# Kernel optimization log

Hardware: AMD Instinct MI355X
Metric: run time of the kernel (lower is better)

## Reference

```python
import jax, jax.numpy as jnp
import numpy as np

NUM_NODES = 100000
NUM_EDGES = 3200000
NUM_GRAPHS = 512
IN_DIM, OUT_DIM = 128, 16
DIMS = [IN_DIM, 32, 48, 64]


def glorot(key, shape):
    lim = float(np.sqrt(6.0 / (shape[0] + shape[1])))
    return jax.random.uniform(key, shape, jnp.float32, -lim, lim)


def setup_inputs() -> dict:
    key = jax.random.key(0)
    ks = jax.random.split(key, 12)
    x = jax.random.normal(ks[0], (NUM_NODES, IN_DIM), jnp.float32)
    edge_index = jax.random.randint(ks[1], (2, NUM_EDGES), 0, NUM_NODES, jnp.int64)
    batch = jnp.sort(jax.random.randint(ks[2], (NUM_NODES,), 0, NUM_GRAPHS, jnp.int64))
    params = {}
    for i in range(3):
        params[f"W{i+1}"] = glorot(ks[3 + i], (DIMS[i], DIMS[i + 1]))
        params[f"b{i+1}"] = jnp.zeros((DIMS[i + 1],), jnp.float32)
    params["fc1_w"] = glorot(ks[6], (64, 32))
    params["fc1_b"] = jnp.zeros((32,), jnp.float32)
    params["fc2_w"] = glorot(ks[7], (32, OUT_DIM))
    params["fc2_b"] = jnp.zeros((OUT_DIM,), jnp.float32)
    return {"x": x, "edge_index": edge_index, "batch": batch, **params}


def gcn_conv(x, W, b, src, dst, deg_inv_sqrt):
    # h = x @ W; aggregate with symmetric normalization + self loops (PyG GCNConv)
    h = x @ W  # [N, out]
    norm = deg_inv_sqrt[src] * deg_inv_sqrt[dst]  # [E]
    msg = h[src] * norm[:, None]  # [E, out]  (gather)
    agg = jnp.zeros_like(h).at[dst].add(msg)  # scatter-add to targets
    self_loop = h * (deg_inv_sqrt * deg_inv_sqrt)[:, None]
    return agg + self_loop + b


def reference(x, edge_index, batch, W1, b1, W2, b2, W3, b3, fc1_w, fc1_b, fc2_w, fc2_b):
    src, dst = edge_index[0], edge_index[1]
    n = x.shape[0]
    # degree with self loops: deg[i] = in-degree + 1
    deg = jnp.zeros((n,), jnp.float32).at[dst].add(1.0) + 1.0
    dis = jax.lax.rsqrt(deg)
    h = jax.nn.relu(gcn_conv(x, W1, b1, src, dst, dis))
    h = jax.nn.relu(gcn_conv(h, W2, b2, src, dst, dis))
    h = jax.nn.relu(gcn_conv(h, W3, b3, src, dst, dis))
    # global mean pool per graph
    sums = jax.ops.segment_sum(h, batch, num_segments=NUM_GRAPHS)
    cnts = jax.ops.segment_sum(jnp.ones((n,), jnp.float32), batch, num_segments=NUM_GRAPHS)
    pooled = sums / jnp.maximum(cnts, 1.0)[:, None]  # [G, 64]
    z = jax.nn.relu(pooled @ fc1_w + fc1_b)
    logits = z @ fc2_w + fc2_b
    return jax.nn.softmax(logits, axis=1)
```

## Files before the change

### kernel.cpp

```cpp
#include <hip/hip_runtime.h>
#include <hip/hip_fp16.h>

static constexpr int NN = 100000;
static constexpr int NE = 3200000;
static constexpr int NG = 512;
static constexpr int NCB = 196;
static constexpr int CHK = 8192;
static constexpr int NCH = (NE + CHK - 1) / CHK;
static constexpr int NCNT = NCB * NCH;
static constexpr int SCAN_BLK = 2048;
static constexpr int NSB = (NCNT + SCAN_BLK - 1) / SCAN_BLK;

typedef float f32x2 __attribute__((ext_vector_type(2)));

__device__ __forceinline__ void set2_fp8x4(unsigned v, f32x2* a) {
    a[0] = __builtin_amdgcn_cvt_pk_f32_fp8((int)v, false);
    a[1] = __builtin_amdgcn_cvt_pk_f32_fp8((int)v, true);
}
__device__ __forceinline__ void acc2_fp8x4(unsigned v, f32x2* a) {
    a[0] += __builtin_amdgcn_cvt_pk_f32_fp8((int)v, false);
    a[1] += __builtin_amdgcn_cvt_pk_f32_fp8((int)v, true);
}
__device__ __forceinline__ unsigned pack_fp8x4(float a, float b, float c, float d) {
    int p = __builtin_amdgcn_cvt_pk_fp8_f32(a, b, 0, false);
    p = __builtin_amdgcn_cvt_pk_fp8_f32(c, d, p, true);
    return (unsigned)p;
}
__device__ __forceinline__ unsigned pkh2(float a, float b) {
    __half2 h = __floats2half2_rn(a, b);
    return *(unsigned*)&h;
}

__global__ __launch_bounds__(256) void k_histC(const int4* __restrict__ dst4,
                                               int* __restrict__ cntC, int e4) {
    __shared__ int h[NCB];
    for (int i = threadIdx.x; i < NCB; i += 256) h[i] = 0;
    __syncthreads();
    const int s4 = blockIdx.x * (CHK / 4), e4end = min(s4 + CHK / 4, e4);
    for (int i = s4 + threadIdx.x; i < e4end; i += 256) {
        int4 d = dst4[i];
        atomicAdd(&h[d.x >> 9], 1);
        atomicAdd(&h[d.y >> 9], 1);
        atomicAdd(&h[d.z >> 9], 1);
        atomicAdd(&h[d.w >> 9], 1);
    }
    __syncthreads();
    for (int i = threadIdx.x; i < NCB; i += 256)
        cntC[(size_t)i * NCH + blockIdx.x] = h[i];
}

__global__ __launch_bounds__(256) void k_scanA(const int* __restrict__ in,
                                               int* __restrict__ out,
                                               int* __restrict__ bsum, int n) {
    __shared__ int s[256];
    const int tid = threadIdx.x;
    const int base = blockIdx.x * SCAN_BLK + tid * 8;
    int v[8], t = 0;
#pragma unroll
    for (int c = 0; c < 8; c++) {
        int idx = base + c;
        v[c] = (idx < n) ? in[idx] : 0;
        t += v[c];
    }
    s[tid] = t;
    __syncthreads();
    for (int off = 1; off < 256; off <<= 1) {
        int x = (tid >= off) ? s[tid - off] : 0;
        __syncthreads();
        s[tid] += x;
        __syncthreads();
    }
    if (tid == 255) bsum[blockIdx.x] = s[255];
    int run = s[tid] - t;
#pragma unroll
    for (int c = 0; c < 8; c++) {
        int idx = base + c;
        if (idx < n) out[idx] = run;
        run += v[c];
    }
}

__global__ __launch_bounds__(256) void k_scanB(int* __restrict__ bsum, int nb) {
    __shared__ int s[256];
    const int tid = threadIdx.x;
    int v = (tid < nb) ? bsum[tid] : 0;
    s[tid] = v;
    __syncthreads();
    for (int off = 1; off < 256; off <<= 1) {
        int x = (tid >= off) ? s[tid - off] : 0;
        __syncthreads();
        s[tid] += x;
        __syncthreads();
    }
    if (tid < nb) bsum[tid] = s[tid] - v;
}

__global__ __launch_bounds__(256) void k_scatC(const int4* __restrict__ src4,
                                               const int4* __restrict__ dst4,
                                               const int* __restrict__ sc,
                                               const int* __restrict__ bsum,
                                               unsigned* __restrict__ tmp, int e4) {
    __shared__ int cur[NCB];
    for (int i = threadIdx.x; i < NCB; i += 256) {
        size_t idx = (size_t)i * NCH + blockIdx.x;
        cur[i] = sc[idx] + bsum[idx >> 11];
    }
    __syncthreads();
    const int s4 = blockIdx.x * (CHK / 4), e4end = min(s4 + CHK / 4, e4);
    for (int i = s4 + threadIdx.x; i < e4end; i += 256) {
        int4 d = dst4[i];
        int4 sv = src4[i];
        int p0 = atomicAdd(&cur[d.x >> 9], 1);
        tmp[p0] = ((unsigned)(d.x & 511) << 17) | (unsigned)sv.x;
        int p1 = atomicAdd(&cur[d.y >> 9], 1);
        tmp[p1] = ((unsigned)(d.y & 511) << 17) | (unsigned)sv.y;
        int p2 = atomicAdd(&cur[d.z >> 9], 1);
        tmp[p2] = ((unsigned)(d.z & 511) << 17) | (unsigned)sv.z;
        int p3 = atomicAdd(&cur[d.w >> 9], 1);
        tmp[p3] = ((unsigned)(d.w & 511) << 17) | (unsigned)sv.w;
    }
}

__global__ __launch_bounds__(1024) void k_fill512(const unsigned* __restrict__ tmp,
                                                  const int* __restrict__ sc,
                                                  const int* __restrict__ bsum,
                                                  int* __restrict__ csr,
                                                  int* __restrict__ degi,
                                                  int* __restrict__ offs,
                                                  float* __restrict__ dis,
                                                  int n, int etotal) {
    __shared__ int cnt[512];
    __shared__ int s[512];
    __shared__ int cur[512];
    const int b = blockIdx.x, tid = threadIdx.x;
    if (tid < 512) cnt[tid] = 0;
    size_t i0 = (size_t)b * NCH;
    const int e0 = sc[i0] + bsum[i0 >> 11];
    int e1 = etotal;
    if (b + 1 < NCB) {
        size_t i1 = (size_t)(b + 1) * NCH;
        e1 = sc[i1] + bsum[i1 >> 11];
    }
    __syncthreads();
    for (int e = e0 + tid; e < e1; e += 1024)
        atomicAdd(&cnt[tmp[e] >> 17], 1);
    __syncthreads();
    int v = 0;
    if (tid < 512) { v = cnt[tid]; s[tid] = v; }
    __syncthreads();
    for (int off = 1; off < 512; off <<= 1) {
        int x = 0;
        if (tid < 512 && tid >= off) x = s[tid - off];
        __syncthreads();
        if (tid < 512) s[tid] += x;
        __syncthreads();
    }
    if (tid < 512) {
        int c = e0 + s[tid] - v;
        cur[tid] = c;
        int node = b * 512 + tid;
        if (node < n) {
            degi[node] = v;
            offs[node] = c;
            dis[node] = rsqrtf((float)v + 1.0f);
        }
    }
    __syncthreads();
    for (int e = e0 + tid; e < e1; e += 1024) {
        unsigned pk = tmp[e];
        int p = atomicAdd(&cur[pk >> 17], 1);
        csr[p] = (int)(pk & 0x1FFFFu);
    }
}

__global__ __launch_bounds__(256) void k_gemm1(const float* __restrict__ X,
                                               const float* __restrict__ W,
                                               const float* __restrict__ dis,
                                               unsigned* __restrict__ H, int n) {
    constexpr int IN = 128, ROWS = 32;
    __shared__ float sW[IN * 32];
    __shared__ float sX[ROWS][IN];
    const int tid = threadIdx.x;
    for (int i = tid; i < IN * 32; i += 256) sW[i] = W[i];
    const int row0 = blockIdx.x * ROWS;
    const float4* X4 = (const float4*)X;
    for (int i = tid; i < ROWS * 32; i += 256) {
        int r = row0 + (i >> 5);
        float4 v = make_float4(0.f, 0.f, 0.f, 0.f);
        if (r < n) v = X4[(size_t)r * 32 + (i & 31)];
        ((float4*)&sX[i >> 5][0])[i & 31] = v;
    }
    __syncthreads();
    const int lr = tid >> 3;
    const int cg = tid & 7;
    const int gr = row0 + lr;
    float acc[4] = {0.f, 0.f, 0.f, 0.f};
#pragma unroll 8
    for (int k = 0; k < IN; k++) {
        float xv = sX[lr][k];
#pragma unroll
        for (int c = 0; c < 4; c++)
            acc[c] = fmaf(xv, sW[k * 32 + 4 * cg + c], acc[c]);
    }
    if (gr < n) {
        float dd = dis[gr];
        H[(size_t)gr * 8 + cg] =
            pack_fp8x4(acc[0] * dd, acc[1] * dd, acc[2] * dd, acc[3] * dd);
    }
}

__global__ __launch_bounds__(256) void k_pull2(
        const uint2* __restrict__ Hp, const int* __restrict__ offs,
        const int* __restrict__ degi, const int* __restrict__ csr,
        const float* __restrict__ dis, const float* __restrict__ b,
        uint2* __restrict__ A, int n) {
    const int group = threadIdx.x >> 2, j0 = threadIdx.x & 3;
    const int d = blockIdx.x * 64 + group;
    if (d >= n) return;
    f32x2 acc[4];
    uint2 sv = Hp[(size_t)d * 4 + j0];
    set2_fp8x4(sv.x, acc); set2_fp8x4(sv.y, acc + 2);
    int e = offs[d];
    const int end = e + degi[d];
    for (; e < end; e += 8) {
        uint2 v[8];
#pragma unroll
        for (int i = 0; i < 8; i++) {
            int ee = e + i;
            int idx = csr[min(ee, NE - 1)];
            uint2 t = Hp[(size_t)idx * 4 + j0];
            if (ee >= end) { t.x = 0u; t.y = 0u; }
            v[i] = t;
        }
#pragma unroll
        for (int i = 0; i < 8; i++) {
            acc2_fp8x4(v[i].x, acc); acc2_fp8x4(v[i].y, acc + 2);
        }
    }
    const float dd = dis[d];
    float r[8];
#pragma unroll
    for (int c = 0; c < 4; c++) {
        r[2 * c]     = fmaxf(fmaf(acc[c].x, dd, b[8 * j0 + 2 * c]), 0.f) * dd;
        r[2 * c + 1] = fmaxf(fmaf(acc[c].y, dd, b[8 * j0 + 2 * c + 1]), 0.f) * dd;
    }
    A[(size_t)d * 4 + j0] = make_uint2(pack_fp8x4(r[0], r[1], r[2], r[3]),
                                       pack_fp8x4(r[4], r[5], r[6], r[7]));
}

__global__ __launch_bounds__(256) void k_pullmm32(
        const uint2* __restrict__ Hp, const int* __restrict__ offs,
        const int* __restrict__ degi, const int* __restrict__ csr,
        const float* __restrict__ dis, const float* __restrict__ W,
        const float* __restrict__ b, unsigned* __restrict__ A, int n) {
    __shared__ float sW[32 * 48];
    __shared__ float rows[64][33];
    for (int i = threadIdx.x; i < 32 * 48; i += 256) sW[i] = W[i];
    const int group = threadIdx.x >> 2, j0 = threadIdx.x & 3;
    const int d = blockIdx.x * 64 + group;
    if (d < n) {
        f32x2 acc[4];
        uint2 sv = Hp[(size_t)d * 4 + j0];
        set2_fp8x4(sv.x, acc); set2_fp8x4(sv.y, acc + 2);
        int e = offs[d];
        const int end = e + degi[d];
        for (; e < end; e += 8) {
            uint2 v[8];
#pragma unroll
            for (int i = 0; i < 8; i++) {
                int ee = e + i;
                int idx = csr[min(ee, NE - 1)];
                uint2 t = Hp[(size_t)idx * 4 + j0];
                if (ee >= end) { t.x = 0u; t.y = 0u; }
                v[i] = t;
            }
#pragma unroll
            for (int i = 0; i < 8; i++) {
                acc2_fp8x4(v[i].x, acc); acc2_fp8x4(v[i].y, acc + 2);
            }
        }
        const float dd = dis[d];
#pragma unroll
        for (int c = 0; c < 4; c++) {
            rows[group][8 * j0 + 2 * c]     = acc[c].x * dd;
            rows[group][8 * j0 + 2 * c + 1] = acc[c].y * dd;
        }
    }
    __syncthreads();
    const int row0 = blockIdx.x * 64;
    const int nl = threadIdx.x & 63, cgb = threadIdx.x >> 6;
    const int gr = row0 + nl;
    if (gr < n) {
        const float4* sW4 = (const float4*)sW;
        float s[3][4];
#pragma unroll
        for (int o = 0; o < 3; o++)
#pragma unroll
            for (int c = 0; c < 4; c++) s[o][c] = b[12 * cgb + 4 * o + c];
#pragma unroll 8
        for (int k = 0; k < 32; k++) {
            float rv = rows[nl][k];
#pragma unroll
            for (int o = 0; o < 3; o++) {
                float4 w = sW4[k * 12 + cgb * 3 + o];
                s[o][0] = fmaf(rv, w.x, s[o][0]);
                s[o][1] = fmaf(rv, w.y, s[o][1]);
                s[o][2] = fmaf(rv, w.z, s[o][2]);
                s[o][3] = fmaf(rv, w.w, s[o][3]);
            }
        }
        const float dd2 = dis[gr];
#pragma unroll
        for (int o = 0; o < 3; o++) {
            float r0 = fmaxf(s[o][0], 0.f) * dd2;
            float r1 = fmaxf(s[o][1], 0.f) * dd2;
            float r2 = fmaxf(s[o][2], 0.f) * dd2;
            float r3 = fmaxf(s[o][3], 0.f) * dd2;
            A[(size_t)gr * 12 + cgb * 3 + o] = pack_fp8x4(r0, r1, r2, r3);
        }
    }
}

__global__ __launch_bounds__(256) void k_pullmm48(
        const uint4* __restrict__ Hp,
        const int* __restrict__ offs,
        const int* __restrict__ degi, const int* __restrict__ csr,
        const float* __restrict__ dis, const float* __restrict__ W,
        const float* __restrict__ b, __half* __restrict__ A, int n) {
    __shared__ float sW[48 * 64];
    __shared__ float rows[64][49];
    for (int i = threadIdx.x; i < 48 * 64; i += 256) sW[i] = W[i];
    const int group = threadIdx.x >> 2, j0 = threadIdx.x & 3;
    const int d = blockIdx.x * 64 + group;
    if (d < n && j0 < 3) {
        f32x2 acc[8];
        uint4 sv = Hp[(size_t)d * 3 + j0];
        set2_fp8x4(sv.x, acc);     set2_fp8x4(sv.y, acc + 2);
        set2_fp8x4(sv.z, acc + 4); set2_fp8x4(sv.w, acc + 6);
        int e = offs[d];
        const int end = e + degi[d];
        for (; e < end; e += 8) {
            uint4 v[8];
#pragma unroll
            for (int i = 0; i < 8; i++) {
                int ee = e + i;
                int idx = csr[min(ee, NE - 1)];
                uint4 t = Hp[(size_t)idx * 3 + j0];
                if (ee >= end) { t.x = 0u; t.y = 0u; t.z = 0u; t.w = 0u; }
                v[i] = t;
            }
#pragma unroll
            for (int i = 0; i < 8; i++) {
                acc2_fp8x4(v[i].x, acc);     acc2_fp8x4(v[i].y, acc + 2);
                acc2_fp8x4(v[i].z, acc + 4); acc2_fp8x4(v[i].w, acc + 6);
            }
        }
        const float dd = dis[d];
#pragma unroll
        for (int c = 0; c < 8; c++) {
            rows[group][16 * j0 + 2 * c]     = acc[c].x * dd;
            rows[group][16 * j0 + 2 * c + 1] = acc[c].y * dd;
        }
    }
    __syncthreads();
    const int row0 = blockIdx.x * 64;
    const int nl = threadIdx.x & 63, cgb = threadIdx.x >> 6;
    const int gr = row0 + nl;
    if (gr < n) {
        const float4* sW4 = (const float4*)sW;
        float s[4][4];
#pragma unroll
        for (int o = 0; o < 4; o++)
#pragma unroll
            for (int c = 0; c < 4; c++) s[o][c] = b[16 * cgb + 4 * o + c];
#pragma unroll 8
        for (int k = 0; k < 48; k++) {
            float rv = rows[nl][k];
#pragma unroll
            for (int o = 0; o < 4; o++) {
                float4 w = sW4[k * 16 + cgb * 4 + o];
                s[o][0] = fmaf(rv, w.x, s[o][0]);
                s[o][1] = fmaf(rv, w.y, s[o][1]);
                s[o][2] = fmaf(rv, w.z, s[o][2]);
                s[o][3] = fmaf(rv, w.w, s[o][3]);
            }
        }
        uint4 q0, q1;
        q0.x = pkh2(s[0][0], s[0][1]); q0.y = pkh2(s[0][2], s[0][3]);
        q0.z = pkh2(s[1][0], s[1][1]); q0.w = pkh2(s[1][2], s[1][3]);
        q1.x = pkh2(s[2][0], s[2][1]); q1.y = pkh2(s[2][2], s[2][3]);
        q1.z = pkh2(s[3][0], s[3][1]); q1.w = pkh2(s[3][2], s[3][3]);
        ((uint4*)A)[(size_t)gr * 8 + cgb * 2]     = q0;
        ((uint4*)A)[(size_t)gr * 8 + cgb * 2 + 1] = q1;
    }
}

__global__ __launch_bounds__(256) void k_poolhead(
        const __half* __restrict__ A3, const int* __restrict__ batch,
        const float* __restrict__ f1w, const float* __restrict__ f1b,
        const float* __restrict__ f2w, const float* __restrict__ f2b,
        float* __restrict__ out, int n, int ngr) {
    const int g = blockIdx.x;
    __shared__ int sb[2];
    if (threadIdx.x < 2) {
        int target = g + threadIdx.x;
        int lo = 0, hi = n;
        while (lo < hi) {
            int mid = (lo + hi) >> 1;
            if (batch[mid] < target) lo = mid + 1; else hi = mid;
        }
        sb[threadIdx.x] = lo;
    }
    __syncthreads();
    const int s = sb[0], e = sb[1];
    const int j = threadIdx.x & 63, rl = threadIdx.x >> 6;
    float sum = 0.f;
    for (int node = s + rl; node < e; node += 4)
        sum += fmaxf(__half2float(A3[(size_t)node * 64 + j]), 0.f);
    __shared__ float red[4][64];
    __shared__ float p[64], z[32], lg[16];
    red[rl][j] = sum;
    __syncthreads();
    if (rl == 0)
        p[j] = (red[0][j] + red[1][j] + red[2][j] + red[3][j]) /
               fmaxf((float)(e - s), 1.f);
    __syncthreads();
    const int t = threadIdx.x;
    if (t < 32) {
        float acc = f1b[t];
        for (int k = 0; k < 64; k++) acc = fmaf(p[k], f1w[k * 32 + t], acc);
        z[t] = fmaxf(acc, 0.f);
    }
    __syncthreads();
    if (t < 16) {
        float acc = f2b[t];
        for (int k = 0; k < 32; k++) acc = fmaf(z[k], f2w[k * 16 + t], acc);
        lg[t] = acc;
    }
    __syncthreads();
    if (t < 16) {
        float m = lg[0];
        for (int i = 1; i < 16; i++) m = fmaxf(m, lg[i]);
        float sden = 0.f;
        for (int i = 0; i < 16; i++) sden += expf(lg[i] - m);
        out[g * 16 + t] = expf(lg[t] - m) / sden;
    }
}

extern "C" void kernel_launch(void* const* d_in, const int* in_sizes, int n_in,
                              void* d_out, int out_size, void* d_ws, size_t ws_size,
                              hipStream_t stream) {
    (void)in_sizes; (void)n_in; (void)out_size; (void)ws_size;
    const float* x     = (const float*)d_in[0];
    const int*   ei    = (const int*)d_in[1];
    const int*   batch = (const int*)d_in[2];
    const float* W1 = (const float*)d_in[3];
    const float* b1 = (const float*)d_in[4];
    const float* W2 = (const float*)d_in[5];  const float* b2 = (const float*)d_in[6];
    const float* W3 = (const float*)d_in[7];  const float* b3 = (const float*)d_in[8];
    const float* f1w = (const float*)d_in[9]; const float* f1b = (const float*)d_in[10];
    const float* f2w = (const float*)d_in[11];const float* f2b = (const float*)d_in[12];
    float* out = (float*)d_out;

    const int* src = ei;
    const int* dst = ei + NE;

    float* ws = (float*)d_ws;
    size_t o = 0;
    float* dis    = ws + o; o += NN;
    int*   degi   = (int*)(ws + o); o += NN;
    int*   offs   = (int*)(ws + o); o += NN;
    int*   cntC   = (int*)(ws + o); o += 76640;
    int*   sc     = (int*)(ws + o); o += 76640;
    int*   bsum   = (int*)(ws + o); o += 48;
    int*   csr    = (int*)(ws + o); o += NE;
    unsigned* TA  = (unsigned*)(ws + o); o += NE;
    unsigned* H1  = (unsigned*)(ws + o); o += NN * 8;
    unsigned* H2  = (unsigned*)(ws + o); o += NN * 8;
    unsigned* H3  = (unsigned*)(ws + o); o += NN * 12;

    unsigned* tmp = (unsigned*)TA;
    __half*   A3  = (__half*)TA;

    k_histC<<<NCH, 256, 0, stream>>>((const int4*)dst, cntC, NE / 4);
    k_scanA<<<NSB, 256, 0, stream>>>(cntC, sc, bsum, NCNT);
    k_scanB<<<1, 256, 0, stream>>>(bsum, NSB);
    k_scatC<<<NCH, 256, 0, stream>>>((const int4*)src, (const int4*)dst,
                                     sc, bsum, tmp, NE / 4);
    k_fill512<<<NCB, 1024, 0, stream>>>(tmp, sc, bsum, csr, degi, offs, dis, NN, NE);

    const int PGRID = (NN + 63) / 64;

    k_gemm1<<<(NN + 31) / 32, 256, 0, stream>>>(x, W1, dis, H1, NN);
    k_pull2<<<PGRID, 256, 0, stream>>>((const uint2*)H1, offs, degi, csr, dis, b1,
                                       (uint2*)H2, NN);

    k_pullmm32<<<PGRID, 256, 0, stream>>>((const uint2*)H2, offs, degi, csr, dis,
                                          W2, b2, H3, NN);

    k_pullmm48<<<PGRID, 256, 0, stream>>>(
        (const uint4*)H3, offs, degi, csr, dis, W3, b3, A3, NN);

    k_poolhead<<<NG, 256, 0, stream>>>(A3, batch, f1w, f1b, f2w, f2b, out, NN, NG);
}
```

Before: 336.3 us.

## Sort nodes by descending degree to balance work in pull kernels

Builds a degree histogram in the CSR fill kernel, scans it, and scatters node ids into a permutation ordered by descending in-degree. The three pull/aggregate kernels then process nodes in this order, so each wavefront handles nodes with similar degree and the high-degree nodes start first. This targets divergence inside wavefronts and tail imbalance in the edge loops. It adds a memset, a scan and a scatter kernel, plus an extra indirection. Reads and writes of node rows become non-contiguous, which reduces coalescing.

Result: slower. 572.9 us (+70.4%).

```diff
diff --git a/kernel.cpp b/kernel.cpp
--- a/kernel.cpp
+++ b/kernel.cpp
@@ -128,6 +128,7 @@
                                                   int* __restrict__ degi,
                                                   int* __restrict__ offs,
                                                   float* __restrict__ dis,
+                                                  int* __restrict__ dcnt,
                                                   int n, int etotal) {
     __shared__ int cnt[512];
     __shared__ int s[512];
@@ -163,6 +164,7 @@
             degi[node] = v;
             offs[node] = c;
             dis[node] = rsqrtf((float)v + 1.0f);
+            atomicAdd(&dcnt[255 - min(v, 255)], 1);
         }
     }
     __syncthreads();
@@ -171,6 +173,25 @@
         int p = atomicAdd(&cur[pk >> 17], 1);
         csr[p] = (int)(pk & 0x1FFFFu);
     }
+}
+
+__global__ __launch_bounds__(256) void k_dscat(const int* __restrict__ degi,
+                                               int* __restrict__ dbase,
+                                               int* __restrict__ perm, int n) {
+    __shared__ int h[256], base[256];
+    h[threadIdx.x] = 0;
+    __syncthreads();
+    const int i = blockIdx.x * 256 + threadIdx.x;
+    int k = 0, rank = 0;
+    if (i < n) {
+        k = 255 - min(degi[i], 255);
+        rank = atomicAdd(&h[k], 1);
+    }
+    __syncthreads();
+    if (h[threadIdx.x] > 0)
+        base[threadIdx.x] = atomicAdd(&dbase[threadIdx.x], h[threadIdx.x]);
+    __syncthreads();
+    if (i < n) perm[base[k] + rank] = i;
 }
 
 __global__ __launch_bounds__(256) void k_gemm1(const float* __restrict__ X,
@@ -213,10 +234,11 @@
         const uint2* __restrict__ Hp, const int* __restrict__ offs,
         const int* __restrict__ degi, const int* __restrict__ csr,
         const float* __restrict__ dis, const float* __restrict__ b,
-        uint2* __restrict__ A, int n) {
+        const int* __restrict__ perm, uint2* __restrict__ A, int n) {
     const int group = threadIdx.x >> 2, j0 = threadIdx.x & 3;
-    const int d = blockIdx.x * 64 + group;
-    if (d >= n) return;
+    const int gi = blockIdx.x * 64 + group;
+    if (gi >= n) return;
+    const int d = perm[gi];
     f32x2 acc[4];
     uint2 sv = Hp[(size_t)d * 4 + j0];
     set2_fp8x4(sv.x, acc); set2_fp8x4(sv.y, acc + 2);
@@ -252,13 +274,15 @@
         const uint2* __restrict__ Hp, const int* __restrict__ offs,
         const int* __restrict__ degi, const int* __restrict__ csr,
         const float* __restrict__ dis, const float* __restrict__ W,
-        const float* __restrict__ b, unsigned* __restrict__ A, int n) {
+        const float* __restrict__ b, const int* __restrict__ perm,
+        unsigned* __restrict__ A, int n) {
     __shared__ float sW[32 * 48];
     __shared__ float rows[64][33];
     for (int i = threadIdx.x; i < 32 * 48; i += 256) sW[i] = W[i];
     const int group = threadIdx.x >> 2, j0 = threadIdx.x & 3;
-    const int d = blockIdx.x * 64 + group;
-    if (d < n) {
+    const int gi = blockIdx.x * 64 + group;
+    if (gi < n) {
+        const int d = perm[gi];
         f32x2 acc[4];
         uint2 sv = Hp[(size_t)d * 4 + j0];
         set2_fp8x4(sv.x, acc); set2_fp8x4(sv.y, acc + 2);
@@ -289,8 +313,9 @@
     __syncthreads();
     const int row0 = blockIdx.x * 64;
     const int nl = threadIdx.x & 63, cgb = threadIdx.x >> 6;
-    const int gr = row0 + nl;
-    if (gr < n) {
+    const int gidx = row0 + nl;
+    if (gidx < n) {
+        const int gr = perm[gidx];
         const float4* sW4 = (const float4*)sW;
         float s[3][4];
 #pragma unroll
@@ -326,13 +351,15 @@
         const int* __restrict__ offs,
         const int* __restrict__ degi, const int* __restrict__ csr,
         const float* __restrict__ dis, const float* __restrict__ W,
-        const float* __restrict__ b, __half* __restrict__ A, int n) {
+        const float* __restrict__ b, const int* __restrict__ perm,
+        __half* __restrict__ A, int n) {
     __shared__ float sW[48 * 64];
     __shared__ float rows[64][49];
     for (int i = threadIdx.x; i < 48 * 64; i += 256) sW[i] = W[i];
     const int group = threadIdx.x >> 2, j0 = threadIdx.x & 3;
-    const int d = blockIdx.x * 64 + group;
-    if (d < n && j0 < 3) {
+    const int gi = blockIdx.x * 64 + group;
+    if (gi < n && j0 < 3) {
+        const int d = perm[gi];
         f32x2 acc[8];
         uint4 sv = Hp[(size_t)d * 3 + j0];
         set2_fp8x4(sv.x, acc);     set2_fp8x4(sv.y, acc + 2);
@@ -365,8 +392,9 @@
     __syncthreads();
     const int row0 = blockIdx.x * 64;
     const int nl = threadIdx.x & 63, cgb = threadIdx.x >> 6;
-    const int gr = row0 + nl;
-    if (gr < n) {
+    const int gidx = row0 + nl;
+    if (gidx < n) {
+        const int gr = perm[gidx];
         const float4* sW4 = (const float4*)sW;
         float s[4][4];
 #pragma unroll
@@ -470,9 +498,11 @@
     float* dis    = ws + o; o += NN;
     int*   degi   = (int*)(ws + o); o += NN;
     int*   offs   = (int*)(ws + o); o += NN;
+    int*   perm   = (int*)(ws + o); o += NN;
     int*   cntC   = (int*)(ws + o); o += 76640;
     int*   sc     = (int*)(ws + o); o += 76640;
     int*   bsum   = (int*)(ws + o); o += 48;
+    int*   dbase  = (int*)(ws + o); o += 256;
     int*   csr    = (int*)(ws + o); o += NE;
     unsigned* TA  = (unsigned*)(ws + o); o += NE;
     unsigned* H1  = (unsigned*)(ws + o); o += NN * 8;
@@ -482,24 +512,29 @@
     unsigned* tmp = (unsigned*)TA;
     __half*   A3  = (__half*)TA;
 
+    hipMemsetAsync(dbase, 0, 256 * sizeof(int), stream);
     k_histC<<<NCH, 256, 0, stream>>>((const int4*)dst, cntC, NE / 4);
     k_scanA<<<NSB, 256, 0, stream>>>(cntC, sc, bsum, NCNT);
     k_scanB<<<1, 256, 0, stream>>>(bsum, NSB);
     k_scatC<<<NCH, 256, 0, stream>>>((const int4*)src, (const int4*)dst,
                                      sc, bsum, tmp, NE / 4);
-    k_fill512<<<NCB, 1024, 0, stream>>>(tmp, sc, bsum, csr, degi, offs, dis, NN, NE);
+    k_fill512<<<NCB, 1024, 0, stream>>>(tmp, sc, bsum, csr, degi, offs, dis,
+                                        dbase, NN, NE);
+
+    k_scanB<<<1, 256, 0, stream>>>(dbase, 256);
+    k_dscat<<<(NN + 255) / 256, 256, 0, stream>>>(degi, dbase, perm, NN);
 
     const int PGRID = (NN + 63) / 64;
 
     k_gemm1<<<(NN + 31) / 32, 256, 0, stream>>>(x, W1, dis, H1, NN);
     k_pull2<<<PGRID, 256, 0, stream>>>((const uint2*)H1, offs, degi, csr, dis, b1,
-                                       (uint2*)H2, NN);
+                                       perm, (uint2*)H2, NN);
 
     k_pullmm32<<<PGRID, 256, 0, stream>>>((const uint2*)H2, offs, degi, csr, dis,
-                                          W2, b2, H3, NN);
+                                          W2, b2, perm, H3, NN);
 
     k_pullmm48<<<PGRID, 256, 0, stream>>>(
-        (const uint4*)H3, offs, degi, csr, dis, W3, b3, A3, NN);
+        (const uint4*)H3, offs, degi, csr, dis, W3, b3, perm, A3, NN);
 
     k_poolhead<<<NG, 256, 0, stream>>>(A3, batch, f1w, f1b, f2w, f2b, out, NN, NG);
 }
```
